# Kernel tuning notes

Hardware: AMD Instinct MI355X
Metric: run time of the kernel (lower is better)

Reference implementation:

```python
import jax, jax.numpy as jnp
import numpy as np

N_V, N_E, N_F = 6000, 12000, 8000
D_IN, D_OUT = 32, 32


def _glorot(key, shape):
    lim = float(np.sqrt(6.0 / (shape[0] + shape[1])))
    return jax.random.uniform(key, shape, jnp.float32, -lim, lim)


def setup_inputs() -> dict:
    key = jax.random.key(0)
    ks = jax.random.split(key, 13)
    return {
        "xv": jax.random.normal(ks[0], (N_V, D_IN), jnp.float32),
        "xe": jax.random.normal(ks[1], (N_E, D_IN), jnp.float32),
        "xf": jax.random.normal(ks[2], (N_F, D_IN), jnp.float32),
        "Gv2v": jax.random.normal(ks[3], (N_V, N_V), jnp.float32) / np.sqrt(N_V),
        "Gv2e": jax.random.normal(ks[4], (N_E, N_V), jnp.float32) / np.sqrt(N_V),
        "Ge2e": jax.random.normal(ks[5], (N_E, N_E), jnp.float32) / np.sqrt(N_E),
        "Ge2f": jax.random.normal(ks[6], (N_F, N_E), jnp.float32) / np.sqrt(N_E),
        "Gf2f": jax.random.normal(ks[7], (N_F, N_F), jnp.float32) / np.sqrt(N_F),
        "Wv2v": _glorot(ks[8], (D_IN, D_OUT)),
        "Wv2e": _glorot(ks[9], (D_IN, D_OUT)),
        "We2e": _glorot(ks[10], (D_IN, D_OUT)),
        "We2f": _glorot(ks[11], (D_IN, D_OUT)),
        "Wf2f": _glorot(ks[12], (D_IN, D_OUT)),
    }


def reference(xv, xe, xf, Gv2v, Gv2e, Ge2e, Ge2f, Gf2f,
              Wv2v, Wv2e, We2e, We2f, Wf2f):
    # Eval mode: dropout is identity. activation=None -> no nonlinearity.
    # LTN(x, G) = G @ (x @ W); MergeOper = sum of two LTNs.
    zv = Gv2v @ (xv @ Wv2v)                               # [n_v, d_out]
    ze = Gv2e @ (xv @ Wv2e) + Ge2e @ (xe @ We2e)          # [n_e, d_out]
    zf = Ge2f @ (xe @ We2f) + Gf2f @ (xf @ Wf2f)          # [n_f, d_out]
    return zv, ze, zf
```

## Files before the change

### kernel.cpp

```cpp
#include <hip/hip_runtime.h>

typedef float  f32x4 __attribute__((ext_vector_type(4)));
typedef short  s16x8 __attribute__((ext_vector_type(8)));

#define PK   256
#define PSTR 260
#define TM   32

typedef const __attribute__((address_space(1))) float* gas1f;
typedef __attribute__((address_space(3))) float*       las3f;

__device__ __forceinline__ short f2bf(float f) {
  unsigned u = __builtin_bit_cast(unsigned, f);
  u += 0x7FFFu + ((u >> 16) & 1u);
  return (short)(u >> 16);
}

__global__ __launch_bounds__(256) void build_yt(
    const float* __restrict__ xv, const float* __restrict__ xe,
    const float* __restrict__ xf,
    const float* __restrict__ Wv2v, const float* __restrict__ Wv2e,
    const float* __restrict__ We2e, const float* __restrict__ We2f,
    const float* __restrict__ Wf2f, short* __restrict__ Yt)
{
  int bid = blockIdx.x;
  const float* x; const float* W; int K, Kpad; size_t yoff;
  if (bid < 24)       { x=xv; W=Wv2v; K=6000;  Kpad=6144;  yoff=0;       }
  else if (bid < 48)  { x=xv; W=Wv2e; K=6000;  Kpad=6144;  yoff=196608;  bid-=24; }
  else if (bid < 95)  { x=xe; W=We2e; K=12000; Kpad=12032; yoff=393216;  bid-=48; }
  else if (bid < 142) { x=xe; W=We2f; K=12000; Kpad=12032; yoff=778240;  bid-=95; }
  else                { x=xf; W=Wf2f; K=8000;  Kpad=8192;  yoff=1163264; bid-=142; }

  __shared__ float Wl[32][32];
  __shared__ short sh[32][264];
  int tid = threadIdx.x;
  #pragma unroll
  for (int i = 0; i < 4; ++i) {
    int e = tid + i * 256;
    Wl[e >> 5][e & 31] = W[e];
  }
  __syncthreads();

  int row = bid * 256 + tid;
  float acc[32];
  #pragma unroll
  for (int c = 0; c < 32; ++c) acc[c] = 0.f;

  if (row < K) {
    const float* xp = x + (size_t)row * 32;
    float xr[32];
    #pragma unroll
    for (int i = 0; i < 8; ++i) {
      f32x4 v = *(const f32x4*)(xp + i * 4);
      xr[i*4+0] = v.x; xr[i*4+1] = v.y; xr[i*4+2] = v.z; xr[i*4+3] = v.w;
    }
    #pragma unroll
    for (int d = 0; d < 32; ++d) {
      float xd = xr[d];
      #pragma unroll
      for (int c = 0; c < 32; ++c) acc[c] += xd * Wl[d][c];
    }
  }
  #pragma unroll
  for (int c = 0; c < 32; ++c) sh[c][tid] = f2bf(acc[c]);
  __syncthreads();

  int c = tid >> 3, q = tid & 7;
  const short* sp = &sh[c][q * 32];
  short* dp = Yt + yoff + (size_t)c * Kpad + (size_t)bid * 256 + q * 32;
  #pragma unroll
  for (int i = 0; i < 4; ++i)
    *(s16x8*)(dp + i * 8) = *(const s16x8*)(sp + i * 8);
}

__device__ __forceinline__ void stage_panel(
    const float* __restrict__ G, int K, int row0, int pn, int lane, int w,
    float (*panel)[TM][PSTR], int bb)
{
  if ((pn + 1) * PK <= K) {
    const float* base = G + (size_t)row0 * K + (size_t)pn * PK;
    #pragma unroll
    for (int j = 0; j < 4; ++j) {
      int rr = 4 * w + j;
      __builtin_amdgcn_global_load_lds((gas1f)(base + (size_t)rr * K + lane * 4),
                                       (las3f)&panel[bb][rr][0], 16, 0, 2 );
    }
  } else {
    #pragma unroll
    for (int j = 0; j < 4; ++j) {
      int rr = 4 * w + j;
      int k = pn * PK + lane * 4;
      f32x4 v = {0.f, 0.f, 0.f, 0.f};
      if (k < K) v = *(const f32x4*)(G + (size_t)(row0 + rr) * K + k);
      *(f32x4*)&panel[bb][rr][lane * 4] = v;
    }
  }
}

__device__ __forceinline__ void loadB(const short* __restrict__ Y, int Kp,
                                      int r, int g, int w, int p, s16x8 B[2])
{
  int kg = p * PK + w * 32 + g * 8;
  B[0] = *(const s16x8*)(Y + (size_t)r        * Kp + kg);
  B[1] = *(const s16x8*)(Y + (size_t)(r + 16) * Kp + kg);
}

__device__ __forceinline__ void seg_run(
    const float* __restrict__ G, const short* __restrict__ Yt,
    int K, int Kp, int row0, int p_lo, int p_hi, int lane, int w,
    float (*panel)[TM][PSTR],
    f32x4& acc00, f32x4& acc01, f32x4& acc10, f32x4& acc11)
{
  if (p_lo >= p_hi) return;
  int r = lane & 15, g = lane >> 4;
  s16x8 Bc[2], Bn[2];

  stage_panel(G, K, row0, p_lo, lane, w, panel, p_lo & 1);
  loadB(Yt, Kp, r, g, w, p_lo, Bc);
  if (p_lo + 1 < p_hi) stage_panel(G, K, row0, p_lo + 1, lane, w, panel, (p_lo + 1) & 1);

  for (int p = p_lo; p < p_hi; ++p) {
    if (p + 1 < p_hi && (p + 2) * PK <= K)
      asm volatile("s_waitcnt vmcnt(4)" ::: "memory");
    else
      asm volatile("s_waitcnt vmcnt(0)" ::: "memory");
    __builtin_amdgcn_s_barrier();

    int b  = p & 1;
    int kk = w * 32 + g * 8;
    f32x4 l0 = *(const f32x4*)&panel[b][r][kk];
    f32x4 l1 = *(const f32x4*)&panel[b][r][kk + 4];
    f32x4 h0 = *(const f32x4*)&panel[b][r + 16][kk];
    f32x4 h1 = *(const f32x4*)&panel[b][r + 16][kk + 4];
    s16x8 alo, ahi;
    alo[0]=f2bf(l0.x); alo[1]=f2bf(l0.y); alo[2]=f2bf(l0.z); alo[3]=f2bf(l0.w);
    alo[4]=f2bf(l1.x); alo[5]=f2bf(l1.y); alo[6]=f2bf(l1.z); alo[7]=f2bf(l1.w);
    ahi[0]=f2bf(h0.x); ahi[1]=f2bf(h0.y); ahi[2]=f2bf(h0.z); ahi[3]=f2bf(h0.w);
    ahi[4]=f2bf(h1.x); ahi[5]=f2bf(h1.y); ahi[6]=f2bf(h1.z); ahi[7]=f2bf(h1.w);
    acc00 = __builtin_amdgcn_mfma_f32_16x16x32_bf16(alo, Bc[0], acc00, 0, 0, 0);
    acc01 = __builtin_amdgcn_mfma_f32_16x16x32_bf16(alo, Bc[1], acc01, 0, 0, 0);
    acc10 = __builtin_amdgcn_mfma_f32_16x16x32_bf16(ahi, Bc[0], acc10, 0, 0, 0);
    acc11 = __builtin_amdgcn_mfma_f32_16x16x32_bf16(ahi, Bc[1], acc11, 0, 0, 0);

    bool have_next = (p + 1 < p_hi);
    if (have_next) loadB(Yt, Kp, r, g, w, p + 1, Bn);

    asm volatile("s_waitcnt lgkmcnt(0)" ::: "memory");
    __builtin_amdgcn_sched_barrier(0);
    __builtin_amdgcn_s_barrier();
    if (p + 2 < p_hi) stage_panel(G, K, row0, p + 2, lane, w, panel, b);

    if (have_next) { Bc[0] = Bn[0]; Bc[1] = Bn[1]; }
  }
  __syncthreads();
}

__global__ __launch_bounds__(512) void gemm_skinny(
    const float* __restrict__ Gv2v, const float* __restrict__ Gv2e,
    const float* __restrict__ Ge2e, const float* __restrict__ Ge2f,
    const float* __restrict__ Gf2f, const short* __restrict__ Yt,
    float* __restrict__ part, float* __restrict__ out)
{
  __shared__ float panel[2][TM][PSTR];

  int bid  = blockIdx.x;
  int lane = threadIdx.x & 63, w = threadIdx.x >> 6;

  const float *Ga, *Gb = nullptr; const short *Ya, *Yb = nullptr;
  int Ka, Kpa, alo, ahi, Kb = 0, Kpb = 0, blo = 0, bhi = 0, tile, row0;
  float* dst;
  if (bid < 250) {
    tile = bid; row0 = tile * TM;
    Ga = Ge2f; Ya = Yt + 778240; Ka = 12000; Kpa = 12032; alo = 0;  ahi = 40;
    dst = out + 576000 + (size_t)tile * 1024;
  } else if (bid < 500) {
    tile = bid - 250; row0 = tile * TM;
    Ga = Ge2f; Ya = Yt + 778240;  Ka = 12000; Kpa = 12032; alo = 40; ahi = 47;
    Gb = Gf2f; Yb = Yt + 1163264; Kb = 8000;  Kpb = 8192;  blo = 0;  bhi = 32;
    dst = part + (size_t)tile * 1024;
  } else if (bid < 875) {
    tile = bid - 500; row0 = tile * TM;
    Ga = Ge2e; Ya = Yt + 393216; Ka = 12000; Kpa = 12032; alo = 11; ahi = 47;
    dst = part + (size_t)(250 + tile) * 1024;
  } else if (bid < 1250) {
    tile = bid - 875; row0 = tile * TM;
    Ga = Gv2e; Ya = Yt + 196608; Ka = 6000;  Kpa = 6144;  alo = 0; ahi = 24;
    Gb = Ge2e; Yb = Yt + 393216; Kb = 12000; Kpb = 12032; blo = 0; bhi = 11;
    dst = out + 192000 + (size_t)tile * 1024;
  } else {
    tile = bid - 1250; row0 = tile * TM;
    if (row0 + TM > 6000) row0 = 6000 - TM;
    Ga = Gv2v; Ya = Yt; Ka = 6000; Kpa = 6144; alo = 0; ahi = 24;
    dst = out + (size_t)row0 * 32;
  }

  f32x4 acc00 = {0.f,0.f,0.f,0.f}, acc01 = {0.f,0.f,0.f,0.f};
  f32x4 acc10 = {0.f,0.f,0.f,0.f}, acc11 = {0.f,0.f,0.f,0.f};
  seg_run(Ga, Ya, Ka, Kpa, row0, alo, ahi, lane, w, panel,
          acc00, acc01, acc10, acc11);
  if (Gb)
    seg_run(Gb, Yb, Kb, Kpb, row0, blo, bhi, lane, w, panel,
            acc00, acc01, acc10, acc11);

  float (*red)[1024] = (float (*)[1024])panel;
  int r = lane & 15, g = lane >> 4;
  #pragma unroll
  for (int q = 0; q < 4; ++q) {
    int rl = g * 4 + q;
    red[w][ rl       * 32 +      r] = acc00[q];
    red[w][ rl       * 32 + 16 + r] = acc01[q];
    red[w][(rl + 16) * 32 +      r] = acc10[q];
    red[w][(rl + 16) * 32 + 16 + r] = acc11[q];
  }
  __syncthreads();
  #pragma unroll
  for (int i = 0; i < 2; ++i) {
    int e = (int)threadIdx.x + i * 512;
    float s = red[0][e] + red[1][e] + red[2][e] + red[3][e]
            + red[4][e] + red[5][e] + red[6][e] + red[7][e];
    dst[e] = s;
  }
}

__global__ __launch_bounds__(256) void reduce_partials(
    float* __restrict__ out, const float* __restrict__ part)
{
  int e = blockIdx.x * 256 + threadIdx.x;
  if (e < 256000) {
    out[576000 + e] += part[e];
  } else {
    int e2 = e - 256000;
    out[192000 + e2] += part[256000 + e2];
  }
}

extern "C" void kernel_launch(void* const* d_in, const int* in_sizes, int n_in,
                              void* d_out, int out_size, void* d_ws, size_t ws_size,
                              hipStream_t stream) {
  const float* xv   = (const float*)d_in[0];
  const float* xe   = (const float*)d_in[1];
  const float* xf   = (const float*)d_in[2];
  const float* Gv2v = (const float*)d_in[3];
  const float* Gv2e = (const float*)d_in[4];
  const float* Ge2e = (const float*)d_in[5];
  const float* Ge2f = (const float*)d_in[6];
  const float* Gf2f = (const float*)d_in[7];
  const float* Wv2v = (const float*)d_in[8];
  const float* Wv2e = (const float*)d_in[9];
  const float* We2e = (const float*)d_in[10];
  const float* We2f = (const float*)d_in[11];
  const float* Wf2f = (const float*)d_in[12];
  short* Yt   = (short*)d_ws;
  float* part = (float*)((char*)d_ws + 2850816);
  float* out  = (float*)d_out;

  hipLaunchKernelGGL(build_yt, dim3(174), dim3(256), 0, stream,
                     xv, xe, xf, Wv2v, Wv2e, We2e, We2f, Wf2f, Yt);
  hipLaunchKernelGGL(gemm_skinny, dim3(1438), dim3(512), 0, stream,
                     Gv2v, Gv2e, Ge2e, Ge2f, Gf2f, Yt, part, out);
  hipLaunchKernelGGL(reduce_partials, dim3(2500), dim3(256), 0, stream,
                     out, part);
}
```

Measured before the change: 294.9 us.

## Rebalance split-K block assignment into three roughly equal K chunks per tile

The skinny GEMM's work split is repartitioned. Each output row tile of the ze and zf outputs is now covered by three interleaved blocks with roughly equal K-panel counts (about 24–27 panels each), where before each tile had two blocks of unequal length. The grid grows to 2063 blocks, and the partials buffer doubles to two slices per tile, which the reduce kernel sums together. The aim is better load balance and a smaller tail wave. In exchange there is extra partial-sum traffic and a larger workspace requirement.

```diff
diff --git a/kernel.cpp b/kernel.cpp
--- a/kernel.cpp
+++ b/kernel.cpp
@@ -169,26 +169,33 @@
   const float *Ga, *Gb = nullptr; const short *Ya, *Yb = nullptr;
   int Ka, Kpa, alo, ahi, Kb = 0, Kpb = 0, blo = 0, bhi = 0, tile, row0;
   float* dst;
-  if (bid < 250) {
-    tile = bid; row0 = tile * TM;
-    Ga = Ge2f; Ya = Yt + 778240; Ka = 12000; Kpa = 12032; alo = 0;  ahi = 40;
-    dst = out + 576000 + (size_t)tile * 1024;
-  } else if (bid < 500) {
-    tile = bid - 250; row0 = tile * TM;
-    Ga = Ge2f; Ya = Yt + 778240;  Ka = 12000; Kpa = 12032; alo = 40; ahi = 47;
-    Gb = Gf2f; Yb = Yt + 1163264; Kb = 8000;  Kpb = 8192;  blo = 0;  bhi = 32;
-    dst = part + (size_t)tile * 1024;
-  } else if (bid < 875) {
-    tile = bid - 500; row0 = tile * TM;
-    Ga = Ge2e; Ya = Yt + 393216; Ka = 12000; Kpa = 12032; alo = 11; ahi = 47;
-    dst = part + (size_t)(250 + tile) * 1024;
-  } else if (bid < 1250) {
-    tile = bid - 875; row0 = tile * TM;
-    Ga = Gv2e; Ya = Yt + 196608; Ka = 6000;  Kpa = 6144;  alo = 0; ahi = 24;
-    Gb = Ge2e; Yb = Yt + 393216; Kb = 12000; Kpb = 12032; blo = 0; bhi = 11;
-    dst = out + 192000 + (size_t)tile * 1024;
+  if (bid < 750) {
+    tile = bid / 3; int c = bid - tile * 3; row0 = tile * TM;
+    if (c == 0) {
+      Ga = Ge2f; Ya = Yt + 778240; Ka = 12000; Kpa = 12032; alo = 0;  ahi = 27;
+      dst = out + 576000 + (size_t)tile * 1024;
+    } else if (c == 1) {
+      Ga = Ge2f; Ya = Yt + 778240;  Ka = 12000; Kpa = 12032; alo = 27; ahi = 47;
+      Gb = Gf2f; Yb = Yt + 1163264; Kb = 8000;  Kpb = 8192;  blo = 0;  bhi = 6;
+      dst = part + (size_t)(tile * 2) * 1024;
+    } else {
+      Ga = Gf2f; Ya = Yt + 1163264; Ka = 8000; Kpa = 8192; alo = 6; ahi = 32;
+      dst = part + (size_t)(tile * 2 + 1) * 1024;
+    }
+  } else if (bid < 1875) {
+    int t2 = bid - 750; tile = t2 / 3; int c = t2 - tile * 3; row0 = tile * TM;
+    if (c == 0) {
+      Ga = Gv2e; Ya = Yt + 196608; Ka = 6000; Kpa = 6144; alo = 0; ahi = 24;
+      dst = out + 192000 + (size_t)tile * 1024;
+    } else if (c == 1) {
+      Ga = Ge2e; Ya = Yt + 393216; Ka = 12000; Kpa = 12032; alo = 0; ahi = 24;
+      dst = part + (size_t)(500 + tile * 2) * 1024;
+    } else {
+      Ga = Ge2e; Ya = Yt + 393216; Ka = 12000; Kpa = 12032; alo = 24; ahi = 47;
+      dst = part + (size_t)(500 + tile * 2 + 1) * 1024;
+    }
   } else {
-    tile = bid - 1250; row0 = tile * TM;
+    tile = bid - 1875; row0 = tile * TM;
     if (row0 + TM > 6000) row0 = 6000 - TM;
     Ga = Gv2v; Ya = Yt; Ka = 6000; Kpa = 6144; alo = 0; ahi = 24;
     dst = out + (size_t)row0 * 32;
@@ -227,10 +234,14 @@
 {
   int e = blockIdx.x * 256 + threadIdx.x;
   if (e < 256000) {
-    out[576000 + e] += part[e];
+    int t = e >> 10, wi = e & 1023;
+    const float* p = part + (size_t)(t * 2) * 1024;
+    out[576000 + e] += p[wi] + p[1024 + wi];
   } else {
     int e2 = e - 256000;
-    out[192000 + e2] += part[256000 + e2];
+    int t = e2 >> 10, wi = e2 & 1023;
+    const float* p = part + (size_t)(500 + t * 2) * 1024;
+    out[192000 + e2] += p[wi] + p[1024 + wi];
   }
 }
 
@@ -256,7 +267,7 @@
 
   hipLaunchKernelGGL(build_yt, dim3(174), dim3(256), 0, stream,
                      xv, xe, xf, Wv2v, Wv2e, We2e, We2f, Wf2f, Yt);
-  hipLaunchKernelGGL(gemm_skinny, dim3(1438), dim3(512), 0, stream,
+  hipLaunchKernelGGL(gemm_skinny, dim3(2063), dim3(512), 0, stream,
                      Gv2v, Gv2e, Ge2e, Ge2f, Gf2f, Yt, part, out);
   hipLaunchKernelGGL(reduce_partials, dim3(2500), dim3(256), 0, stream,
                      out, part);
```

After: 309.5 us. 1.05x slower.
